# Optimization experiments

Hardware: AMD Instinct MI355X
Metric: run time of the kernel (lower is better)

Reference implementation:

```python
import jax, jax.numpy as jnp
import numpy as np

B, N, IN_DIM, HID, K = 8, 4096, 10, 64, 8
NORM = np.array([1.0/2950.0, 1.0/2950.0, 1.0/2950.0, 1.0/5.265625, 1.0/143.875,
                 1.0/589.0, 1.0/1.2050781, 1.0/211.0, 1.0, 1.0/7.0], dtype=np.float32)


def _lin(key, fan_in, fan_out):
    k1, k2 = jax.random.split(key)
    s = 1.0 / np.sqrt(fan_in)
    w = jax.random.uniform(k1, (fan_in, fan_out), jnp.float32, -s, s)
    b = jax.random.uniform(k2, (fan_out,), jnp.float32, -s, s)
    return w, b


def setup_inputs() -> dict:
    key = jax.random.key(0)
    ks = jax.random.split(key, 10)
    x = jax.random.normal(ks[0], (B, N, IN_DIM), jnp.float32)
    w_in1, b_in1 = _lin(ks[1], IN_DIM, HID // 2)
    w_in2, b_in2 = _lin(ks[2], HID // 2, HID)
    w_c1a, b_c1a = _lin(ks[3], 2 * HID, 3 * HID // 2)
    w_c1b, b_c1b = _lin(ks[4], 3 * HID // 2, HID)
    w_c2a, b_c2a = _lin(ks[5], 2 * HID, 3 * HID // 2)
    w_c2b, b_c2b = _lin(ks[6], 3 * HID // 2, HID)
    w_o1, b_o1 = _lin(ks[7], HID, HID)
    w_o2, b_o2 = _lin(ks[8], HID, HID // 2)
    w_o3, b_o3 = _lin(ks[9], HID // 2, 2)
    return dict(x=x, datanorm=jnp.asarray(NORM),
                w_in1=w_in1, b_in1=b_in1, w_in2=w_in2, b_in2=b_in2,
                w_c1a=w_c1a, b_c1a=b_c1a, w_c1b=w_c1b, b_c1b=b_c1b,
                w_c2a=w_c2a, b_c2a=b_c2a, w_c2b=w_c2b, b_c2b=b_c2b,
                w_o1=w_o1, b_o1=b_o1, w_o2=w_o2, b_o2=b_o2, w_o3=w_o3, b_o3=b_o3)


def _knn(x, k):
    # x: [B, n, H] -> [B, n, k] indices of k nearest neighbors (self excluded)
    x2 = jnp.sum(x * x, -1)
    d = x2[:, :, None] + x2[:, None, :] - 2.0 * jnp.einsum('bnh,bmh->bnm', x, x)
    n = x.shape[1]
    d = d + jnp.eye(n, dtype=x.dtype) * 1e9
    return jax.lax.top_k(-d, k)[1]


def _edge_conv(x, nbr, w1, b1, w2, b2):
    # EdgeConv with max aggregation over undirected kNN edges.
    # message(i <- j) = MLP([x_i, x_j - x_i]); edges symmetrized (j->i and i->j).
    b, n, k = nbr.shape
    dst0 = jnp.broadcast_to(jnp.arange(n)[None, :, None], (b, n, k)).reshape(b, n * k)
    src0 = nbr.reshape(b, n * k)
    src = jnp.concatenate([src0, dst0], 1)  # [b, 2nk]
    dst = jnp.concatenate([dst0, src0], 1)
    xd = jnp.take_along_axis(x, dst[..., None], 1)
    xs = jnp.take_along_axis(x, src[..., None], 1)
    m = jnp.concatenate([xd, xs - xd], -1)           # [b, 2nk, 2H]
    m = jax.nn.elu(m @ w1 + b1)
    m = jax.nn.elu(m @ w2 + b2)
    seg = lambda mm, dd: jax.ops.segment_max(mm, dd, num_segments=n)
    return jax.vmap(seg)(m, dst)                     # [b, n, H]


def reference(x, datanorm, w_in1, b_in1, w_in2, b_in2,
              w_c1a, b_c1a, w_c1b, b_c1b, w_c2a, b_c2a, w_c2b, b_c2b,
              w_o1, b_o1, w_o2, b_o2, w_o3, b_o3):
    h = x * datanorm
    h = jax.nn.elu(h @ w_in1 + b_in1)
    h = jax.nn.elu(h @ w_in2 + b_in2)
    nbr = _knn(jax.lax.stop_gradient(h), K)          # knn_graph is non-differentiable
    h = _edge_conv(h, nbr, w_c1a, b_c1a, w_c1b, b_c1b)
    # deterministic pairwise max-pool (stand-in for graclus+max_pool, halves node count)
    h = h.reshape(B, N // 2, 2, HID).max(2)
    nbr = _knn(jax.lax.stop_gradient(h), K)
    h = _edge_conv(h, nbr, w_c2a, b_c2a, w_c2b, b_c2b)
    # second graclus max_pool_x followed by global_max_pool == global max pool
    g = h.max(1)                                     # [B, HID]
    o = jax.nn.elu(g @ w_o1 + b_o1)
    o = jax.nn.elu(o @ w_o2 + b_o2)
    o = o @ w_o3 + b_o3                              # [B, 2]
    met = jax.nn.softplus(o[:, :1])
    metphi = jnp.pi * (2.0 * jax.nn.sigmoid(o[:, 1:2]) - 1.0)
    return jnp.concatenate([met, metphi], 1)
```

## Files before the change

kernel.cpp:

```cpp
#include <hip/hip_runtime.h>
#include <hip/hip_bf16.h>

#define BATCH 8
#define N1 4096
#define N2 2048
#define HID 64
#define KNN 8
#define INDIM 10

using u64 = unsigned long long;
using bf16 = __hip_bfloat16;
typedef __attribute__((ext_vector_type(8))) short short8;
typedef __attribute__((ext_vector_type(4))) float f32x4;

__device__ __align__(256) float    g_h1[BATCH * N1 * HID];
__device__ __align__(256) float    g_h2[BATCH * N2 * HID];
__device__ __align__(256) float    g_x2n[BATCH * N1];
__device__ __align__(256) float    g_x2n2[BATCH * N2];
__device__ __align__(256) int      g_nbr[BATCH * N1 * KNN];
__device__ __align__(256) float    g_uu[BATCH * N1 * 96];
__device__ __align__(256) float    g_vv[BATCH * N1 * 96];
__device__ __align__(256) unsigned g_ek1[BATCH * N1 * HID];
__device__ __align__(256) unsigned g_ek2[BATCH * N2 * HID];
__device__ __align__(256) short    g_f1[BATCH * N1 * HID];
__device__ __align__(256) short    g_f2[BATCH * N1 * HID];
__device__ __align__(256) short    g_f3[BATCH * N1 * HID];
__device__ __align__(256) float    g_uf[BATCH * N1 * 96];
__device__ __align__(256) float    g_vf[BATCH * N1 * 96];
__device__ __align__(256) short    g_wf1[2 * 4 * 3 * 64 * 8];
__device__ __align__(256) short    g_wf2[2 * 4 * 3 * 64 * 8];

__device__ __forceinline__ float eluf(float x) { return x > 0.f ? x : __expf(x) - 1.f; }
__device__ __forceinline__ unsigned encf(float f) {
  unsigned u = __float_as_uint(f);
  return u ^ ((unsigned)((int)u >> 31) | 0x80000000u);
}
__device__ __forceinline__ float decf(unsigned k) {
  unsigned u = (k & 0x80000000u) ? (k & 0x7FFFFFFFu) : ~k;
  return __uint_as_float(u);
}
#define ENC_NEG1 0x407FFFFFu
__device__ __forceinline__ unsigned enc_safe(float v) {
  if (!(v == v)) return ENC_NEG1;
  return encf(v);
}
__device__ __forceinline__ float dec_safe(unsigned k) {
  float v = decf(k);
  if (!(v == v)) return -1.0f;
  return fminf(fmaxf(v, -3.0e38f), 3.0e38f);
}
__device__ __forceinline__ unsigned umed3(unsigned a, unsigned b, unsigned c) {
  unsigned d;
  asm("v_med3_u32 %0, %1, %2, %3" : "=v"(d) : "v"(a), "v"(b), "v"(c));
  return d;
}
__device__ __forceinline__ void split3(float v, short& b1, short& b2, short& b3) {
  bf16 x1 = __float2bfloat16(v);
  float r1 = v - __bfloat162float(x1);
  bf16 x2 = __float2bfloat16(r1);
  float r2 = r1 - __bfloat162float(x2);
  bf16 x3 = __float2bfloat16(r2);
  b1 = *(short*)&x1; b2 = *(short*)&x2; b3 = *(short*)&x3;
}
__device__ __forceinline__ void split2(float v, short& b1, short& b2) {
  bf16 x1 = __float2bfloat16(v);
  float r1 = v - __bfloat162float(x1);
  bf16 x2 = __float2bfloat16(r1);
  b1 = *(short*)&x1; b2 = *(short*)&x2;
}
__device__ __forceinline__ void store_frags(int node, const short* s1,
                                            const short* s2, const short* s3) {
  size_t tb = ((size_t)(node >> 4)) * 1024 + (node & 15) * 8;
#pragma unroll
  for (int chunk = 0; chunk < 2; ++chunk) {
#pragma unroll
    for (int q = 0; q < 4; ++q) {
      size_t a = tb + chunk * 512 + q * 128;
      int k = chunk * 32 + q * 8;
      *(short8*)(g_f1 + a) = *(const short8*)(s1 + k);
      *(short8*)(g_f2 + a) = *(const short8*)(s2 + k);
      *(short8*)(g_f3 + a) = *(const short8*)(s3 + k);
    }
  }
}
__device__ __forceinline__ void tv_frag(float4 a0, float4 a1, float4 b0,
                                        float4 b1, short8& s1, short8& s2) {
  float v[8] = {a0.x + b0.x, a0.y + b0.y, a0.z + b0.z, a0.w + b0.w,
                a1.x + b1.x, a1.y + b1.y, a1.z + b1.z, a1.w + b1.w};
#pragma unroll
  for (int e = 0; e < 8; ++e) {
    float t = eluf(v[e]);
    short p1, p2;
    split2(t, p1, p2);
    s1[e] = p1; s2[e] = p2;
  }
}

__global__ __launch_bounds__(256) void prep_kernel(
    const float* __restrict__ x, const float* __restrict__ norm,
    const float* __restrict__ w1g, const float* __restrict__ b1g,
    const float* __restrict__ w2g, const float* __restrict__ b2g,
    const float* __restrict__ wc1b, const float* __restrict__ wc2b) {
  int bid = blockIdx.x;
  int t = threadIdx.x;
  if (bid < 128) {
    __shared__ float sw1[320], sb1[32], sw2[2048], sb2[64], snorm[INDIM];
    for (int q = t; q < 320; q += 256) sw1[q] = w1g[q];
    for (int q = t; q < 2048; q += 256) sw2[q] = w2g[q];
    if (t < 32) sb1[t] = b1g[t];
    if (t < 64) sb2[t] = b2g[t];
    if (t < INDIM) snorm[t] = norm[t];
    __syncthreads();
    int node = bid * 256 + t;
    float xv[INDIM];
#pragma unroll
    for (int d = 0; d < INDIM; ++d)
      xv[d] = x[(size_t)node * INDIM + d] * snorm[d];
    float t1[32];
#pragma unroll
    for (int c = 0; c < 32; ++c) {
      float acc = sb1[c];
#pragma unroll
      for (int d = 0; d < INDIM; ++d) acc += xv[d] * sw1[d * 32 + c];
      t1[c] = eluf(acc);
    }
    float* hr = g_h1 + (size_t)node * HID;
    float sq = 0.f;
    short s1l[HID], s2l[HID], s3l[HID];
#pragma unroll
    for (int c = 0; c < HID; ++c) {
      float acc = sb2[c];
#pragma unroll
      for (int d = 0; d < 32; ++d) acc += t1[d] * sw2[d * HID + c];
      float v = eluf(acc);
      hr[c] = v;
      sq += v * v;
      split3(v, s1l[c], s2l[c], s3l[c]);
    }
    store_frags(node, s1l, s2l, s3l);
    g_x2n[node] = sq;
  } else if (bid < 130) {
    int level = bid - 128;
    const float* w = level ? wc2b : wc1b;
    for (int idx = t; idx < 6144; idx += 256) {
      int no = idx / 1536;
      int rem = idx - no * 1536;
      int kc = rem / 512;
      int rem2 = rem - kc * 512;
      int lane = rem2 >> 3;
      int j = rem2 & 7;
      int k = kc * 32 + (lane >> 4) * 8 + j;
      int o = no * 16 + (lane & 15);
      short b1, b2;
      split2(w[k * 64 + o], b1, b2);
      g_wf1[level * 6144 + idx] = b1;
      g_wf2[level * 6144 + idx] = b2;
    }
  } else {
    int tt = (bid - 130) * 256 + t;
    uint4 z = make_uint4(ENC_NEG1, ENC_NEG1, ENC_NEG1, ENC_NEG1);
    const int n1 = BATCH * N1 * HID / 4;
    if (tt < n1) ((uint4*)g_ek1)[tt] = z;
    else ((uint4*)g_ek2)[tt - n1] = z;
  }
}

template <int LEVEL>
__device__ __forceinline__ void knn_body(unsigned* lm) {
  constexpr int n = LEVEL ? N2 : N1;
  constexpr int NT = n / 16;
  constexpr int HT = NT / 2;
  constexpr int NSET = LEVEL ? 1 : 2;
  constexpr int SS = NSET * 16;

  int b = blockIdx.x & 7;
  int rb = (blockIdx.x >> 3) * (2 * SS);
  int t = threadIdx.x;
  int wv = t >> 6, lane = t & 63;
  int s = wv >> 1, hf = wv & 1;
  int q = lane >> 4, c = lane & 15;
  const float* __restrict__ x2b = (LEVEL ? g_x2n2 : g_x2n) + (size_t)b * n;
  size_t abase = ((size_t)((b * n + rb + s * SS) >> 4)) * 1024 + lane * 8;
  short8 A1a[NSET], A1b[NSET], A2a[NSET], A2b[NSET], A3a[NSET], A3b[NSET];
#pragma unroll
  for (int e = 0; e < NSET; ++e) {
    size_t ab = abase + (size_t)e * 1024;
    A1a[e] = *(const short8*)(g_f1 + ab);
    A1b[e] = *(const short8*)(g_f1 + ab + 512);
    A2a[e] = *(const short8*)(g_f2 + ab);
    A2b[e] = *(const short8*)(g_f2 + ab + 512);
    A3a[e] = *(const short8*)(g_f3 + ab);
    A3b[e] = *(const short8*)(g_f3 + ab + 512);
  }
  unsigned best[NSET][4][KNN];
#pragma unroll
  for (int e = 0; e < NSET; ++e)
#pragma unroll
    for (int r = 0; r < 4; ++r)
#pragma unroll
      for (int p = 0; p < KNN; ++p) best[e][r][p] = 0xFFFFFFFFu;
  const int ct0 = hf * HT;
  const int selftile = (rb + s * SS) >> 4;
  const f32x4 zero = {0.f, 0.f, 0.f, 0.f};
  size_t bb = ((size_t)(b * n) >> 4) * 1024 + (size_t)ct0 * 1024 + lane * 8;

  short8 Pa[6], Pb[6];
  float xa, xb;
  auto LOADB = [&](short8* P, size_t addr) {
    P[0] = *(const short8*)(g_f1 + addr);
    P[1] = *(const short8*)(g_f1 + addr + 512);
    P[2] = *(const short8*)(g_f2 + addr);
    P[3] = *(const short8*)(g_f2 + addr + 512);
    P[4] = *(const short8*)(g_f3 + addr);
    P[5] = *(const short8*)(g_f3 + addr + 512);
  };
  auto COMPUTE = [&](const short8* P, float x2c, int ct) {
#pragma unroll
    for (int e = 0; e < NSET; ++e) {
      f32x4 acc0 = __builtin_amdgcn_mfma_f32_16x16x32_bf16(A1a[e], P[0], zero, 0, 0, 0);
      f32x4 acc1 = __builtin_amdgcn_mfma_f32_16x16x32_bf16(A1b[e], P[1], zero, 0, 0, 0);
      acc0 = __builtin_amdgcn_mfma_f32_16x16x32_bf16(A1a[e], P[2], acc0, 0, 0, 0);
      acc1 = __builtin_amdgcn_mfma_f32_16x16x32_bf16(A1b[e], P[3], acc1, 0, 0, 0);
      acc0 = __builtin_amdgcn_mfma_f32_16x16x32_bf16(A2a[e], P[0], acc0, 0, 0, 0);
      acc1 = __builtin_amdgcn_mfma_f32_16x16x32_bf16(A2b[e], P[1], acc1, 0, 0, 0);
      acc0 = __builtin_amdgcn_mfma_f32_16x16x32_bf16(A1a[e], P[4], acc0, 0, 0, 0);
      acc1 = __builtin_amdgcn_mfma_f32_16x16x32_bf16(A1b[e], P[5], acc1, 0, 0, 0);
      acc0 = __builtin_amdgcn_mfma_f32_16x16x32_bf16(A2a[e], P[2], acc0, 0, 0, 0);
      acc1 = __builtin_amdgcn_mfma_f32_16x16x32_bf16(A2b[e], P[3], acc1, 0, 0, 0);
      acc0 = __builtin_amdgcn_mfma_f32_16x16x32_bf16(A3a[e], P[0], acc0, 0, 0, 0);
      acc1 = __builtin_amdgcn_mfma_f32_16x16x32_bf16(A3b[e], P[1], acc1, 0, 0, 0);
      unsigned ck[4];
#pragma unroll
      for (int r = 0; r < 4; ++r) {
        float sm2 = acc0[r] + acc1[r];
        float dd = __builtin_fmaf(-2.f, sm2, x2c);
        ck[r] = (encf(dd) & 0xFFFFFF00u) | (unsigned)ct;
      }
      if (ct == selftile + e) {
#pragma unroll
        for (int r = 0; r < 4; ++r)
          if (c == q * 4 + r) ck[r] = 0xFFFFFFFFu;
      }
#pragma unroll
      for (int r = 0; r < 4; ++r) {
        unsigned x = ck[r];
#pragma unroll
        for (int p = KNN - 1; p >= 1; --p)
          best[e][r][p] = umed3(best[e][r][p - 1], best[e][r][p], x);
        best[e][r][0] = min(best[e][r][0], x);
      }
    }
  };

  LOADB(Pa, bb);
  xa = x2b[ct0 * 16 + c];
  for (int tt = 0; tt < HT; tt += 2) {
    int ct = ct0 + tt;
    LOADB(Pb, bb + 1024);
    xb = x2b[(ct + 1) * 16 + c];
    COMPUTE(Pa, xa, ct);
    size_t nb2 = (tt + 2 < HT) ? bb + 2048 : bb;
    int ctn2 = (tt + 2 < HT) ? ct + 2 : ct;
    LOADB(Pa, nb2);
    xa = x2b[ctn2 * 16 + c];
    COMPUTE(Pb, xb, ct + 1);
    bb += 2048;
  }
#pragma unroll
  for (int pass = 0; pass < NSET; ++pass) {
#pragma unroll
    for (int r = 0; r < 4; ++r) {
      int lrow = s * 16 + q * 4 + r;
      unsigned* dst = lm + lrow * 289 + (hf * 16 + c) * 9;
#pragma unroll
      for (int p = 0; p < KNN; ++p) dst[p] = best[pass][r][p];
    }
    __syncthreads();
    {
      int arow = t >> 3, am = t & 7;
      unsigned* base = lm + arow * 289;
      const unsigned* l0 = base + (am * 4) * 9;
      u64 fin[KNN];
#pragma unroll
      for (int p = 0; p < KNN; ++p)
        fin[p] = (((u64)l0[p]) << 4) | (unsigned)((am * 4) & 15);
      for (int d = 1; d < 4; ++d) {
        const unsigned* ld = base + (am * 4 + d) * 9;
        unsigned cb = (unsigned)((am * 4 + d) & 15);
        for (int p = 0; p < KNN; ++p) {
          u64 ckk = (((u64)ld[p]) << 4) | cb;
          if (ckk >= fin[KNN - 1]) break;
#pragma unroll
          for (int p2 = 0; p2 < KNN; ++p2) {
            u64 ob = fin[p2];
            bool ex = ob < ckk;
            fin[p2] = ex ? ob : ckk;
            ckk = ex ? ckk : ob;
          }
        }
      }
      unsigned* dst = base + (am * 4) * 9;
#pragma unroll
      for (int p = 0; p < KNN; ++p) {
        dst[2 * p] = (unsigned)fin[p];
        dst[2 * p + 1] = (unsigned)(fin[p] >> 32);
      }
    }
    __syncthreads();
    if (t < 64) {
      int brow = t >> 1, bm = t & 1;
      unsigned* base = lm + brow * 289;
      u64 fin[KNN];
      {
        const unsigned* s0 = base + (bm * 4) * 36;
#pragma unroll
        for (int p = 0; p < KNN; ++p)
          fin[p] = (((u64)s0[2 * p + 1]) << 32) | s0[2 * p];
      }
      for (int d = 1; d < 4; ++d) {
        const unsigned* sd = base + (bm * 4 + d) * 36;
        for (int p = 0; p < KNN; ++p) {
          u64 ckk = (((u64)sd[2 * p + 1]) << 32) | sd[2 * p];
          if (ckk >= fin[KNN - 1]) break;
#pragma unroll
          for (int p2 = 0; p2 < KNN; ++p2) {
            u64 ob = fin[p2];
            bool ex = ob < ckk;
            fin[p2] = ex ? ob : ckk;
            ckk = ex ? ckk : ob;
          }
        }
      }
      unsigned* dst = base + (bm * 4) * 36;
#pragma unroll
      for (int p = 0; p < KNN; ++p) {
        dst[2 * p] = (unsigned)fin[p];
        dst[2 * p + 1] = (unsigned)(fin[p] >> 32);
      }
    }
    __syncthreads();
    if (t < 32) {
      unsigned* base = lm + t * 289;
      u64 fin[KNN];
#pragma unroll
      for (int p = 0; p < KNN; ++p)
        fin[p] = (((u64)base[2 * p + 1]) << 32) | base[2 * p];
      const unsigned* s1 = base + 144;
      for (int p = 0; p < KNN; ++p) {
        u64 ckk = (((u64)s1[2 * p + 1]) << 32) | s1[2 * p];
        if (ckk >= fin[KNN - 1]) break;
#pragma unroll
        for (int p2 = 0; p2 < KNN; ++p2) {
          u64 ob = fin[p2];
          bool ex = ob < ckk;
          fin[p2] = ex ? ob : ckk;
          ckk = ex ? ckk : ob;
        }
      }
      int row = rb + (t >> 4) * SS + pass * 16 + (t & 15);
      int* ob = g_nbr + ((size_t)b * n + row) * KNN;
#pragma unroll
      for (int p = 0; p < KNN; ++p) {
        int j = (int)((fin[p] >> 4) & 255u) * 16 + (int)(fin[p] & 15u);
        ob[p] = j & (n - 1);
      }
    }
    if (pass + 1 < NSET) __syncthreads();
  }
}

template <int LEVEL>
__device__ __forceinline__ void uv_body(float* sw1, float* sb1, int ub,
                                        const float* __restrict__ w1g,
                                        const float* __restrict__ b1g) {
  int t = threadIdx.x;
  for (int q = t; q < 128 * 96; q += 256) sw1[q] = w1g[q];
  if (t < 96) sb1[t] = b1g[t];
  __syncthreads();
  const int n = LEVEL ? N2 : N1;
  const float* h = LEVEL ? g_h2 : g_h1;
  int b = ub & 7;
  int nl = (ub >> 3) * 64 + (t & 63);
  int c0 = (t >> 6) * 24;
  size_t node = (size_t)b * n + nl;
  const float4* h4 = (const float4*)(h + node * HID);
  float ua[24], va[24];
#pragma unroll
  for (int c = 0; c < 24; ++c) { ua[c] = 0.f; va[c] = 0.f; }
  float4 vv = h4[0];
  for (int qd = 0; qd < 16; ++qd) {
    float4 cur = vv;
    if (qd < 15) vv = h4[qd + 1];
    float el[4] = {cur.x, cur.y, cur.z, cur.w};
#pragma unroll
    for (int j = 0; j < 4; ++j) {
      int d = qd * 4 + j;
      float hd = el[j];
      const float* wt = sw1 + d * 96 + c0;
      const float* wb = sw1 + (HID + d) * 96 + c0;
#pragma unroll
      for (int c = 0; c < 24; ++c) {
        ua[c] += hd * wt[c];
        va[c] += hd * wb[c];
      }
    }
  }
  float* ur = g_uu + node * 96 + c0;
  float* vr = g_vv + node * 96 + c0;
#pragma unroll
  for (int c = 0; c < 24; ++c) {
    float uval = ua[c] - va[c] + sb1[c0 + c];
    float vval = va[c];
    ur[c] = uval;
    vr[c] = vval;
    int kk = c0 + c;
    size_t fa = (node >> 4) * 1536 + (size_t)((kk >> 5) * 512 +
                ((kk >> 3) & 3) * 128 + (nl & 15) * 8 + (kk & 7));
    g_uf[fa] = uval;
    g_vf[fa] = vval;
  }
}

template <int LEVEL>
__global__ __launch_bounds__(256, 2) void knuv_kernel(
    const float* __restrict__ w1g, const float* __restrict__ b1g) {
  constexpr int KB = LEVEL ? (8 * (N2 / 32)) : (8 * (N1 / 64));
  __shared__ __align__(16) unsigned char smem[49536];
  if ((int)blockIdx.x < KB) {
    knn_body<LEVEL>((unsigned*)smem);
  } else {
    uv_body<LEVEL>((float*)smem, (float*)(smem + 49152),
                   (int)blockIdx.x - KB, w1g, b1g);
  }
}

template <int LEVEL>
__global__ __launch_bounds__(256, 2) void edge_kernel(
    const float* __restrict__ b2g) {
  constexpr int n = LEVEL ? N2 : N1;
  unsigned* ekey = LEVEL ? g_ek2 : g_ek1;
  __shared__ short sW1[6144], sW2[6144];
  int t = threadIdx.x;
  for (int i = t; i < 768; i += 256) {
    ((short8*)sW1)[i] = ((const short8*)(g_wf1 + LEVEL * 6144))[i];
    ((short8*)sW2)[i] = ((const short8*)(g_wf2 + LEVEL * 6144))[i];
  }
  __syncthreads();
  int b = blockIdx.x & 7;
  int wv = t >> 6, lane = t & 63;
  int q = lane >> 4, c = lane & 15;
  int base16 = (blockIdx.x >> 3) * 64 + wv * 16;
  int node_c = base16 + c;
  const int* nbb = g_nbr + (size_t)b * n * KNN;
  const float* ub = g_uu + (size_t)b * n * 96;
  const float* vb = g_vv + (size_t)b * n * 96;
  size_t ftile = ((size_t)(b * n + base16) >> 4) * 1536;
  unsigned* eb = ekey + (size_t)b * n * HID;
  float biasv[4];
#pragma unroll
  for (int no = 0; no < 4; ++no) biasv[no] = b2g[no * 16 + c];
  int jnl[KNN];
#pragma unroll
  for (int slot = 0; slot < KNN; ++slot)
    jnl[slot] = nbb[(size_t)node_c * KNN + slot] & (n - 1);
  float macc[16];
#pragma unroll
  for (int e = 0; e < 16; ++e) macc[e] = -1.0f;
  for (int slot = 0; slot < KNN; ++slot) {
    int jn = jnl[slot];
    f32x4 aF[4], aR[4];
#pragma unroll
    for (int no = 0; no < 4; ++no) {
      aF[no] = (f32x4){0.f, 0.f, 0.f, 0.f};
      aR[no] = (f32x4){0.f, 0.f, 0.f, 0.f};
    }
#pragma unroll
    for (int kc = 0; kc < 3; ++kc) {
      size_t fo = ftile + kc * 512 + lane * 8;
      float4 su0 = *(const float4*)(g_uf + fo);
      float4 su1 = *(const float4*)(g_uf + fo + 4);
      float4 sv0 = *(const float4*)(g_vf + fo);
      float4 sv1 = *(const float4*)(g_vf + fo + 4);
      size_t go = (size_t)jn * 96 + kc * 32 + q * 8;
      float4 gv0 = *(const float4*)(vb + go);
      float4 gv1 = *(const float4*)(vb + go + 4);
      float4 gu0 = *(const float4*)(ub + go);
      float4 gu1 = *(const float4*)(ub + go + 4);
      short8 t1, t2, r1, r2;
      tv_frag(su0, su1, gv0, gv1, t1, t2);
      tv_frag(gu0, gu1, sv0, sv1, r1, r2);
#pragma unroll
      for (int no = 0; no < 4; ++no) {
        short8 w1 = ((const short8*)sW1)[(no * 3 + kc) * 64 + lane];
        short8 w2 = ((const short8*)sW2)[(no * 3 + kc) * 64 + lane];
        aF[no] = __builtin_amdgcn_mfma_f32_16x16x32_bf16(t1, w1, aF[no], 0, 0, 0);
        aF[no] = __builtin_amdgcn_mfma_f32_16x16x32_bf16(t2, w1, aF[no], 0, 0, 0);
        aF[no] = __builtin_amdgcn_mfma_f32_16x16x32_bf16(t1, w2, aF[no], 0, 0, 0);
        aR[no] = __builtin_amdgcn_mfma_f32_16x16x32_bf16(r1, w1, aR[no], 0, 0, 0);
        aR[no] = __builtin_amdgcn_mfma_f32_16x16x32_bf16(r2, w1, aR[no], 0, 0, 0);
        aR[no] = __builtin_amdgcn_mfma_f32_16x16x32_bf16(r1, w2, aR[no], 0, 0, 0);
      }
    }
#pragma unroll
    for (int r = 0; r < 4; ++r) {
      int jr = nbb[(size_t)(base16 + q * 4 + r) * KNN + slot] & (n - 1);
#pragma unroll
      for (int no = 0; no < 4; ++no) {
        float mv = eluf(aR[no][r] + biasv[no]);
        atomicMax(&eb[(size_t)jr * HID + no * 16 + c], enc_safe(mv));
      }
    }
#pragma unroll
    for (int no = 0; no < 4; ++no)
#pragma unroll
      for (int r = 0; r < 4; ++r)
        macc[no * 4 + r] = fmaxf(macc[no * 4 + r], eluf(aF[no][r] + biasv[no]));
  }
#pragma unroll
  for (int r = 0; r < 4; ++r) {
    size_t ib = (size_t)(base16 + q * 4 + r) * HID;
#pragma unroll
    for (int no = 0; no < 4; ++no)
      atomicMax(&eb[ib + no * 16 + c], enc_safe(macc[no * 4 + r]));
  }
}

__global__ __launch_bounds__(256) void pool_kernel() {
  int node = blockIdx.x * 256 + threadIdx.x;
  int b = node >> 11;
  int m = node & (N2 - 1);
  const unsigned* e = g_ek1 + ((size_t)b * N1 + 2 * m) * HID;
  float* hr = g_h2 + (size_t)node * HID;
  float sq = 0.f;
  short s1l[HID], s2l[HID], s3l[HID];
#pragma unroll
  for (int d = 0; d < HID; ++d) {
    float mx = fmaxf(dec_safe(e[d]), dec_safe(e[HID + d]));
    hr[d] = mx;
    sq += mx * mx;
    split3(mx, s1l[d], s2l[d], s3l[d]);
  }
  store_frags(node, s1l, s2l, s3l);
  g_x2n2[node] = sq;
}

__global__ __launch_bounds__(256) void final_kernel(
    const float* __restrict__ wo1, const float* __restrict__ bo1,
    const float* __restrict__ wo2, const float* __restrict__ bo2,
    const float* __restrict__ wo3, const float* __restrict__ bo3,
    float* __restrict__ out) {
  __shared__ unsigned red[4][HID];
  __shared__ float g[HID];
  __shared__ float o1s[HID];
  __shared__ float o2s[32];
  int b = blockIdx.x;
  int t = threadIdx.x;
  int grp = t >> 6, d = t & 63;
  const unsigned* e = g_ek2 + (size_t)b * N2 * HID;
  unsigned mk = 0u;
  for (int m = grp; m < N2; m += 4) {
    unsigned qv = e[(size_t)m * HID + d];
    mk = qv > mk ? qv : mk;
  }
  red[grp][d] = mk;
  __syncthreads();
  if (t < HID) {
    unsigned q1 = red[0][t] > red[1][t] ? red[0][t] : red[1][t];
    unsigned q2 = red[2][t] > red[3][t] ? red[2][t] : red[3][t];
    g[t] = dec_safe(q1 > q2 ? q1 : q2);
  }
  __syncthreads();
  if (t < HID) {
    float a1 = bo1[t];
    for (int dd = 0; dd < HID; ++dd) a1 += g[dd] * wo1[dd * HID + t];
    o1s[t] = eluf(a1);
  }
  __syncthreads();
  if (t < 32) {
    float a2 = bo2[t];
    for (int dd = 0; dd < HID; ++dd) a2 += o1s[dd] * wo2[dd * 32 + t];
    o2s[t] = eluf(a2);
  }
  __syncthreads();
  if (t == 0) {
    float acc0 = bo3[0];
    float acc1 = bo3[1];
    for (int dd = 0; dd < 32; ++dd) {
      acc0 += o2s[dd] * wo3[dd * 2 + 0];
      acc1 += o2s[dd] * wo3[dd * 2 + 1];
    }
    float met = fmaxf(acc0, 0.f) + log1pf(expf(-fabsf(acc0)));
    float phi = 3.14159265358979f * (2.f / (1.f + expf(-acc1)) - 1.f);
    out[b * 2 + 0] = met;
    out[b * 2 + 1] = phi;
  }
}

extern "C" void kernel_launch(void* const* d_in, const int* in_sizes, int n_in,
                              void* d_out, int out_size, void* d_ws,
                              size_t ws_size, hipStream_t stream) {
  const float* x     = (const float*)d_in[0];
  const float* dnorm = (const float*)d_in[1];
  const float* w_in1 = (const float*)d_in[2];
  const float* b_in1 = (const float*)d_in[3];
  const float* w_in2 = (const float*)d_in[4];
  const float* b_in2 = (const float*)d_in[5];
  const float* w_c1a = (const float*)d_in[6];
  const float* b_c1a = (const float*)d_in[7];
  const float* w_c1b = (const float*)d_in[8];
  const float* b_c1b = (const float*)d_in[9];
  const float* w_c2a = (const float*)d_in[10];
  const float* b_c2a = (const float*)d_in[11];
  const float* w_c2b = (const float*)d_in[12];
  const float* b_c2b = (const float*)d_in[13];
  const float* w_o1  = (const float*)d_in[14];
  const float* b_o1  = (const float*)d_in[15];
  const float* w_o2  = (const float*)d_in[16];
  const float* b_o2  = (const float*)d_in[17];
  const float* w_o3  = (const float*)d_in[18];
  const float* b_o3  = (const float*)d_in[19];

  prep_kernel<<<3202, 256, 0, stream>>>(x, dnorm, w_in1, b_in1, w_in2, b_in2,
                                        w_c1b, w_c2b);
  knuv_kernel<0><<<1024, 256, 0, stream>>>(w_c1a, b_c1a);
  edge_kernel<0><<<8 * (N1 / 64), 256, 0, stream>>>(b_c1b);
  pool_kernel<<<BATCH * N2 / 256, 256, 0, stream>>>();
  knuv_kernel<1><<<768, 256, 0, stream>>>(w_c2a, b_c2a);
  edge_kernel<1><<<8 * (N2 / 64), 256, 0, stream>>>(b_c2b);
  final_kernel<<<BATCH, 256, 0, stream>>>(w_o1, b_o1, w_o2, b_o2, w_o3, b_o3,
                                          (float*)d_out);
}
```

Baseline: 500.8 us.

## Fuse all stages into one persistent kernel with software grid barriers

Replaces the seven kernel launches with a single persistent mega-kernel of 512 blocks that walks through prep, kNN+UV, edge conv, pool, level-2 kNN+UV, edge conv and the final MLP, separated by atomic-counter grid barriers. The aim is to remove per-launch overhead and inter-kernel gaps. It relies on all 512 blocks being co-resident (two per CU at launch bounds 256,2), since otherwise the barrier deadlocks. It also serialises the knn and uv work inside each block where they previously ran as separate concurrent blocks, and leaves many blocks idle in the narrow stages.

```diff
diff --git a/kernel.cpp b/kernel.cpp
--- a/kernel.cpp
+++ b/kernel.cpp
@@ -7,6 +7,7 @@
 #define HID 64
 #define KNN 8
 #define INDIM 10
+#define GRIDN 512
 
 using u64 = unsigned long long;
 using bf16 = __hip_bfloat16;
@@ -29,6 +30,19 @@
 __device__ __align__(256) float    g_vf[BATCH * N1 * 96];
 __device__ __align__(256) short    g_wf1[2 * 4 * 3 * 64 * 8];
 __device__ __align__(256) short    g_wf2[2 * 4 * 3 * 64 * 8];
+__device__ unsigned g_barcnt = 0;
+
+__device__ __forceinline__ void gridbar() {
+  __threadfence();
+  __syncthreads();
+  if (threadIdx.x == 0) {
+    unsigned old = atomicAdd(&g_barcnt, 1u);
+    unsigned target = (old / GRIDN + 1u) * GRIDN;
+    while (atomicAdd(&g_barcnt, 0u) < target) __builtin_amdgcn_s_sleep(8);
+  }
+  __syncthreads();
+  __threadfence();
+}
 
 __device__ __forceinline__ float eluf(float x) { return x > 0.f ? x : __expf(x) - 1.f; }
 __device__ __forceinline__ unsigned encf(float f) {
@@ -96,72 +110,69 @@
   }
 }
 
-__global__ __launch_bounds__(256) void prep_kernel(
-    const float* __restrict__ x, const float* __restrict__ norm,
-    const float* __restrict__ w1g, const float* __restrict__ b1g,
-    const float* __restrict__ w2g, const float* __restrict__ b2g,
-    const float* __restrict__ wc1b, const float* __restrict__ wc2b) {
-  int bid = blockIdx.x;
+__device__ __forceinline__ void mlp_unit(
+    int u, unsigned char* smem, const float* __restrict__ x,
+    const float* __restrict__ norm, const float* __restrict__ w1g,
+    const float* __restrict__ b1g, const float* __restrict__ w2g,
+    const float* __restrict__ b2g) {
+  float* sw1 = (float*)smem;
+  float* sb1 = sw1 + 320;
+  float* sw2 = sb1 + 32;
+  float* sb2 = sw2 + 2048;
+  float* snorm = sb2 + 64;
   int t = threadIdx.x;
-  if (bid < 128) {
-    __shared__ float sw1[320], sb1[32], sw2[2048], sb2[64], snorm[INDIM];
-    for (int q = t; q < 320; q += 256) sw1[q] = w1g[q];
-    for (int q = t; q < 2048; q += 256) sw2[q] = w2g[q];
-    if (t < 32) sb1[t] = b1g[t];
-    if (t < 64) sb2[t] = b2g[t];
-    if (t < INDIM) snorm[t] = norm[t];
-    __syncthreads();
-    int node = bid * 256 + t;
-    float xv[INDIM];
-#pragma unroll
-    for (int d = 0; d < INDIM; ++d)
-      xv[d] = x[(size_t)node * INDIM + d] * snorm[d];
-    float t1[32];
-#pragma unroll
-    for (int c = 0; c < 32; ++c) {
-      float acc = sb1[c];
-#pragma unroll
-      for (int d = 0; d < INDIM; ++d) acc += xv[d] * sw1[d * 32 + c];
-      t1[c] = eluf(acc);
-    }
-    float* hr = g_h1 + (size_t)node * HID;
-    float sq = 0.f;
-    short s1l[HID], s2l[HID], s3l[HID];
-#pragma unroll
-    for (int c = 0; c < HID; ++c) {
-      float acc = sb2[c];
-#pragma unroll
-      for (int d = 0; d < 32; ++d) acc += t1[d] * sw2[d * HID + c];
-      float v = eluf(acc);
-      hr[c] = v;
-      sq += v * v;
-      split3(v, s1l[c], s2l[c], s3l[c]);
-    }
-    store_frags(node, s1l, s2l, s3l);
-    g_x2n[node] = sq;
-  } else if (bid < 130) {
-    int level = bid - 128;
-    const float* w = level ? wc2b : wc1b;
-    for (int idx = t; idx < 6144; idx += 256) {
-      int no = idx / 1536;
-      int rem = idx - no * 1536;
-      int kc = rem / 512;
-      int rem2 = rem - kc * 512;
-      int lane = rem2 >> 3;
-      int j = rem2 & 7;
-      int k = kc * 32 + (lane >> 4) * 8 + j;
-      int o = no * 16 + (lane & 15);
-      short b1, b2;
-      split2(w[k * 64 + o], b1, b2);
-      g_wf1[level * 6144 + idx] = b1;
-      g_wf2[level * 6144 + idx] = b2;
-    }
-  } else {
-    int tt = (bid - 130) * 256 + t;
-    uint4 z = make_uint4(ENC_NEG1, ENC_NEG1, ENC_NEG1, ENC_NEG1);
-    const int n1 = BATCH * N1 * HID / 4;
-    if (tt < n1) ((uint4*)g_ek1)[tt] = z;
-    else ((uint4*)g_ek2)[tt - n1] = z;
+  for (int q = t; q < 320; q += 256) sw1[q] = w1g[q];
+  for (int q = t; q < 2048; q += 256) sw2[q] = w2g[q];
+  if (t < 32) sb1[t] = b1g[t];
+  if (t < 64) sb2[t] = b2g[t];
+  if (t < INDIM) snorm[t] = norm[t];
+  __syncthreads();
+  int node = u * 256 + t;
+  float xv[INDIM];
+#pragma unroll
+  for (int d = 0; d < INDIM; ++d)
+    xv[d] = x[(size_t)node * INDIM + d] * snorm[d];
+  float t1[32];
+#pragma unroll
+  for (int c = 0; c < 32; ++c) {
+    float acc = sb1[c];
+#pragma unroll
+    for (int d = 0; d < INDIM; ++d) acc += xv[d] * sw1[d * 32 + c];
+    t1[c] = eluf(acc);
+  }
+  float* hr = g_h1 + (size_t)node * HID;
+  float sq = 0.f;
+  short s1l[HID], s2l[HID], s3l[HID];
+#pragma unroll
+  for (int c = 0; c < HID; ++c) {
+    float acc = sb2[c];
+#pragma unroll
+    for (int d = 0; d < 32; ++d) acc += t1[d] * sw2[d * HID + c];
+    float v = eluf(acc);
+    hr[c] = v;
+    sq += v * v;
+    split3(v, s1l[c], s2l[c], s3l[c]);
+  }
+  store_frags(node, s1l, s2l, s3l);
+  g_x2n[node] = sq;
+}
+
+__device__ __forceinline__ void wfrag_unit(int level,
+                                           const float* __restrict__ w) {
+  int t = threadIdx.x;
+  for (int idx = t; idx < 6144; idx += 256) {
+    int no = idx / 1536;
+    int rem = idx - no * 1536;
+    int kc = rem / 512;
+    int rem2 = rem - kc * 512;
+    int lane = rem2 >> 3;
+    int j = rem2 & 7;
+    int k = kc * 32 + (lane >> 4) * 8 + j;
+    int o = no * 16 + (lane & 15);
+    short b1, b2;
+    split2(w[k * 64 + o], b1, b2);
+    g_wf1[level * 6144 + idx] = b1;
+    g_wf2[level * 6144 + idx] = b2;
   }
 }
 
@@ -422,24 +433,12 @@
 }
 
 template <int LEVEL>
-__global__ __launch_bounds__(256, 2) void knuv_kernel(
-    const float* __restrict__ w1g, const float* __restrict__ b1g) {
-  constexpr int KB = LEVEL ? (8 * (N2 / 32)) : (8 * (N1 / 64));
-  __shared__ __align__(16) unsigned char smem[49536];
-  if ((int)blockIdx.x < KB) {
-    knn_body<LEVEL>((unsigned*)smem);
-  } else {
-    uv_body<LEVEL>((float*)smem, (float*)(smem + 49152),
-                   (int)blockIdx.x - KB, w1g, b1g);
-  }
-}
-
-template <int LEVEL>
-__global__ __launch_bounds__(256, 2) void edge_kernel(
-    const float* __restrict__ b2g) {
+__device__ __forceinline__ void edge_body(unsigned char* smem,
+                                          const float* __restrict__ b2g) {
   constexpr int n = LEVEL ? N2 : N1;
   unsigned* ekey = LEVEL ? g_ek2 : g_ek1;
-  __shared__ short sW1[6144], sW2[6144];
+  short* sW1 = (short*)smem;
+  short* sW2 = (short*)(smem + 12288);
   int t = threadIdx.x;
   for (int i = t; i < 768; i += 256) {
     ((short8*)sW1)[i] = ((const short8*)(g_wf1 + LEVEL * 6144))[i];
@@ -525,8 +524,8 @@
   }
 }
 
-__global__ __launch_bounds__(256) void pool_kernel() {
-  int node = blockIdx.x * 256 + threadIdx.x;
+__device__ __forceinline__ void pool_unit(int u) {
+  int node = u * 256 + threadIdx.x;
   int b = node >> 11;
   int m = node & (N2 - 1);
   const unsigned* e = g_ek1 + ((size_t)b * N1 + 2 * m) * HID;
@@ -544,16 +543,16 @@
   g_x2n2[node] = sq;
 }
 
-__global__ __launch_bounds__(256) void final_kernel(
+__device__ __forceinline__ void final_body(
+    int b, unsigned char* smem,
     const float* __restrict__ wo1, const float* __restrict__ bo1,
     const float* __restrict__ wo2, const float* __restrict__ bo2,
     const float* __restrict__ wo3, const float* __restrict__ bo3,
     float* __restrict__ out) {
-  __shared__ unsigned red[4][HID];
-  __shared__ float g[HID];
-  __shared__ float o1s[HID];
-  __shared__ float o2s[32];
-  int b = blockIdx.x;
+  unsigned* red = (unsigned*)smem;
+  float* g = (float*)(smem + 1024);
+  float* o1s = (float*)(smem + 1280);
+  float* o2s = (float*)(smem + 1536);
   int t = threadIdx.x;
   int grp = t >> 6, d = t & 63;
   const unsigned* e = g_ek2 + (size_t)b * N2 * HID;
@@ -562,11 +561,12 @@
     unsigned qv = e[(size_t)m * HID + d];
     mk = qv > mk ? qv : mk;
   }
-  red[grp][d] = mk;
+  red[grp * HID + d] = mk;
   __syncthreads();
   if (t < HID) {
-    unsigned q1 = red[0][t] > red[1][t] ? red[0][t] : red[1][t];
-    unsigned q2 = red[2][t] > red[3][t] ? red[2][t] : red[3][t];
+    unsigned q1 = red[t] > red[HID + t] ? red[t] : red[HID + t];
+    unsigned q2 = red[2 * HID + t] > red[3 * HID + t] ? red[2 * HID + t]
+                                                      : red[3 * HID + t];
     g[t] = dec_safe(q1 > q2 ? q1 : q2);
   }
   __syncthreads();
@@ -594,6 +594,53 @@
     out[b * 2 + 0] = met;
     out[b * 2 + 1] = phi;
   }
+}
+
+__global__ __launch_bounds__(256, 2) void mega_kernel(
+    const float* __restrict__ x, const float* __restrict__ dnorm,
+    const float* __restrict__ w_in1, const float* __restrict__ b_in1,
+    const float* __restrict__ w_in2, const float* __restrict__ b_in2,
+    const float* __restrict__ w_c1a, const float* __restrict__ b_c1a,
+    const float* __restrict__ w_c1b, const float* __restrict__ b_c1b,
+    const float* __restrict__ w_c2a, const float* __restrict__ b_c2a,
+    const float* __restrict__ w_c2b, const float* __restrict__ b_c2b,
+    const float* __restrict__ w_o1, const float* __restrict__ b_o1,
+    const float* __restrict__ w_o2, const float* __restrict__ b_o2,
+    const float* __restrict__ w_o3, const float* __restrict__ b_o3,
+    float* __restrict__ out) {
+  __shared__ __align__(16) unsigned char smem[49536];
+  int bid = blockIdx.x;
+
+  for (int u = bid; u < 3202; u += GRIDN) {
+    if (u < 128) {
+      mlp_unit(u, smem, x, dnorm, w_in1, b_in1, w_in2, b_in2);
+    } else if (u < 130) {
+      wfrag_unit(u - 128, (u - 128) ? w_c2b : w_c1b);
+    } else {
+      int tt = (u - 130) * 256 + threadIdx.x;
+      uint4 z = make_uint4(ENC_NEG1, ENC_NEG1, ENC_NEG1, ENC_NEG1);
+      const int n1 = BATCH * N1 * HID / 4;
+      if (tt < n1) ((uint4*)g_ek1)[tt] = z;
+      else ((uint4*)g_ek2)[tt - n1] = z;
+    }
+  }
+  gridbar();
+  knn_body<0>((unsigned*)smem);
+  __syncthreads();
+  uv_body<0>((float*)smem, (float*)(smem + 49152), bid, w_c1a, b_c1a);
+  gridbar();
+  edge_body<0>(smem, b_c1b);
+  gridbar();
+  if (bid < 64) pool_unit(bid);
+  gridbar();
+  knn_body<1>((unsigned*)smem);
+  __syncthreads();
+  if (bid < 256) uv_body<1>((float*)smem, (float*)(smem + 49152), bid,
+                            w_c2a, b_c2a);
+  gridbar();
+  if (bid < 256) edge_body<1>(smem, b_c2b);
+  gridbar();
+  if (bid < 8) final_body(bid, smem, w_o1, b_o1, w_o2, b_o2, w_o3, b_o3, out);
 }
 
 extern "C" void kernel_launch(void* const* d_in, const int* in_sizes, int n_in,
@@ -620,13 +667,8 @@
   const float* w_o3  = (const float*)d_in[18];
   const float* b_o3  = (const float*)d_in[19];
 
-  prep_kernel<<<3202, 256, 0, stream>>>(x, dnorm, w_in1, b_in1, w_in2, b_in2,
-                                        w_c1b, w_c2b);
-  knuv_kernel<0><<<1024, 256, 0, stream>>>(w_c1a, b_c1a);
-  edge_kernel<0><<<8 * (N1 / 64), 256, 0, stream>>>(b_c1b);
-  pool_kernel<<<BATCH * N2 / 256, 256, 0, stream>>>();
-  knuv_kernel<1><<<768, 256, 0, stream>>>(w_c2a, b_c2a);
-  edge_kernel<1><<<8 * (N2 / 64), 256, 0, stream>>>(b_c2b);
-  final_kernel<<<BATCH, 256, 0, stream>>>(w_o1, b_o1, w_o2, b_o2, w_o3, b_o3,
-                                          (float*)d_out);
-}
+  mega_kernel<<<GRIDN, 256, 0, stream>>>(
+      x, dnorm, w_in1, b_in1, w_in2, b_in2, w_c1a, b_c1a, w_c1b, b_c1b,
+      w_c2a, b_c2a, w_c2b, b_c2b, w_o1, b_o1, w_o2, b_o2, w_o3, b_o3,
+      (float*)d_out);
+}
```

Result: slower. 1.208 ms (+141.3%).
